# Kernel optimization log

Measured on AMD Instinct MI355X. Metric: run time of the kernel, lower is better.

The kernel has to match this reference:

```python
import jax, jax.numpy as jnp
import numpy as np
from itertools import permutations

NUM_LAYERS = 3
K = 5  # fixed node degree -> every Hungarian sub-problem is 5x5
# one-hot permutation tensor: P1H[p, r, c] = 1 iff permutation p assigns row r -> col c
PERMS = np.array(list(permutations(range(K))), dtype=np.int32)          # [120, K]
P1H = (PERMS[:, :, None] == np.arange(K)[None, None, :]).astype(np.float32)  # [120, K, K]


def _mlp(x, W1, b1, W2, b2):
    # 2-layer MLP with ReLU (repo's MLP(in, hid, out, 2))
    return jax.nn.relu(x @ W1 + b1) @ W2 + b2


def _sinkhorn(src, itera):
    s = jax.nn.softmax(src, axis=1)  # row-max subtraction is built in
    for i in range(itera):
        s = s / jnp.sum(s, axis=i % 2, keepdims=True)
    return jnp.nan_to_num(s)


def _masked_softmax(src):
    s1 = jnp.nan_to_num(jax.nn.softmax(src, axis=1))
    s2 = jnp.nan_to_num(jax.nn.softmax(src, axis=0))
    return (s1 + s2) * 0.5


def setup_inputs() -> dict:
    key = jax.random.key(0)
    ks = jax.random.split(key, 12)
    n1 = n2 = 1024
    hid = 64
    adj1 = jax.random.randint(ks[0], (n1, K), 0, n1)
    adj2 = jax.random.randint(ks[1], (n2, K), 0, n2)
    # adjacency matrices consistent with the neighbor lists
    G1 = jnp.zeros((n1, n1), jnp.float32).at[jnp.arange(n1)[:, None], adj1].set(1.0)
    G2 = jnp.zeros((n2, n2), jnp.float32).at[jnp.arange(n2)[:, None], adj2].set(1.0)
    s = 0.1
    return {
        'G1': G1, 'G2': G2, 'adj1': adj1, 'adj2': adj2,
        'ro_W1': jax.random.normal(ks[2], (NUM_LAYERS, 1, hid), jnp.float32) * s,
        'ro_b1': jax.random.normal(ks[3], (NUM_LAYERS, hid), jnp.float32) * s,
        'ro_W2': jax.random.normal(ks[4], (NUM_LAYERS, hid, 1), jnp.float32) * s,
        'ro_b2': jax.random.normal(ks[5], (NUM_LAYERS, 1), jnp.float32) * s,
        'fin_W1': jax.random.normal(ks[6], (1, hid), jnp.float32) * s,
        'fin_b1': jax.random.normal(ks[7], (hid,), jnp.float32) * s,
        'fin_W2': jax.random.normal(ks[8], (hid, 1), jnp.float32) * s,
        'fin_b2': jax.random.normal(ks[9], (1,), jnp.float32) * s,
    }


def reference(G1, G2, adj1, adj2, ro_W1, ro_b1, ro_W2, ro_b2, fin_W1, fin_b1, fin_W2, fin_b2):
    n1 = G1.shape[0]
    n2 = G2.shape[0]
    d1 = jnp.sum(G1, axis=1)
    d2 = jnp.sum(G2, axis=1)
    ttheta = jnp.mean(d1)
    # S[i, j, 0] = -|d1[i] - d2[j]|
    S = -jnp.abs(d1[:, None] - d2[None, :])[..., None]  # [n1, n2, 1]
    p1h = jnp.asarray(P1H)
    for li in range(NUM_LAYERS):
        Wn = _sinkhorn(_mlp(S / ttheta, ro_W1[li], ro_b1[li], ro_W2[li], ro_b2[li]).squeeze(-1), 5)
        W = jnp.log(Wn * (n1 * 1.5))
        W = jnp.where(jnp.isneginf(W), jnp.float32(-1e12), W)
        W = jnp.where(jnp.isposinf(W), jnp.float32(1e12), W)
        Wd = jax.lax.stop_gradient(W)  # matches W.detach().numpy()
        # small[a, b, r, c] = Wd[adj1[a, r], adj2[b, c]]  -> [n1, n2, K, K]
        small = jnp.transpose(Wd[adj1][:, :, adj2], (0, 2, 1, 3))
        # exact linear_sum_assignment(-small): maximize sum over the K! permutations
        scores = jnp.einsum('abrc,prc->abp', small, p1h)  # [n1, n2, 120]
        X1 = jnp.max(scores, axis=-1)                      # [n1, n2]
        S = X1[..., None]
    out = _masked_softmax(_mlp(S, fin_W1, fin_b1, fin_W2, fin_b2).squeeze(-1))
    return out
```

## Files before the change

### kernel.cpp

```cpp
#include <hip/hip_runtime.h>
#include <math.h>

#define N 1024
#define NB 256
#define KD 5
#define SL 8
#define NT 126
#define MAGIC 0x13572468
#define FSTRIDE 32
#define FREGION (NB * FSTRIDE + FSTRIDE)


__device__ __forceinline__ float load_sc(const float* p){
  return __hip_atomic_load(p, __ATOMIC_RELAXED, __HIP_MEMORY_SCOPE_AGENT);
}
__device__ __forceinline__ void store_sc(float* p, float v){
  __hip_atomic_store(p, v, __ATOMIC_RELAXED, __HIP_MEMORY_SCOPE_AGENT);
}
__device__ __forceinline__ int load_sci(const int* p){
  return __hip_atomic_load(p, __ATOMIC_RELAXED, __HIP_MEMORY_SCOPE_AGENT);
}
__device__ __forceinline__ void store_sci(int* p, int v){
  __hip_atomic_store(p, v, __ATOMIC_RELAXED, __HIP_MEMORY_SCOPE_AGENT);
}

__device__ __forceinline__ void gbarS(int* flg){
  __builtin_amdgcn_s_waitcnt(0);
  __syncthreads();
  const int t = threadIdx.x, B = blockIdx.x;
  int* go = flg + NB * FSTRIDE;
  if (B == 0){
    if (t > 0 && t < NB){
      while (load_sci(&flg[t * FSTRIDE]) != MAGIC) __builtin_amdgcn_s_sleep(2);
    }
    __syncthreads();
    if (t == 0) store_sci(go, MAGIC);
  } else {
    if (t == 0){
      store_sci(&flg[B * FSTRIDE], MAGIC);
      while (load_sci(go) != MAGIC) __builtin_amdgcn_s_sleep(2);
    }
    __syncthreads();
  }
}

__device__ __forceinline__ float wred_sum(float v){
#pragma unroll
  for (int off = 32; off > 0; off >>= 1) v += __shfl_down(v, off);
  return v;
}
__device__ __forceinline__ void bsum4(float v[4], float* s64){
  float w0 = wred_sum(v[0]), w1 = wred_sum(v[1]), w2 = wred_sum(v[2]), w3 = wred_sum(v[3]);
  __syncthreads();
  int wv = threadIdx.x >> 6;
  if ((threadIdx.x & 63) == 0){ s64[wv*4] = w0; s64[wv*4+1] = w1; s64[wv*4+2] = w2; s64[wv*4+3] = w3; }
  __syncthreads();
  float r0 = 0.f, r1 = 0.f, r2 = 0.f, r3 = 0.f;
#pragma unroll
  for (int i = 0; i < 16; ++i){ r0 += s64[i*4]; r1 += s64[i*4+1]; r2 += s64[i*4+2]; r3 += s64[i*4+3]; }
  v[0] = r0; v[1] = r1; v[2] = r2; v[3] = r3;
}

__device__ __forceinline__ int distinct5(const int* v){
  int c = 0;
#pragma unroll
  for (int r = 0; r < KD; ++r){
    bool dup = false;
#pragma unroll
    for (int s = 0; s < r; ++s) dup = dup || (v[s] == v[r]);
    c += dup ? 0 : 1;
  }
  return c;
}
__device__ __forceinline__ void sort5(int* s){
#pragma unroll
  for (int i = 0; i < 4; ++i)
#pragma unroll
    for (int j = 0; j < 4 - i; ++j){
      int a = s[j], b = s[j+1];
      s[j] = min(a, b); s[j+1] = max(a, b);
    }
}
__device__ __forceinline__ int msrank(const int* c5){
  const int C_[6][5] = { {0,0,0,0,0},
                         {1,1,1,1,1},
                         {1,2,3,4,5},
                         {1,3,6,10,15},
                         {1,4,10,20,35},
                         {1,5,15,35,70} };
  int rank = 0, prev = 0;
#pragma unroll
  for (int i = 0; i < 5; ++i){
    for (int v = prev; v < c5[i]; ++v) rank += C_[5 - v][4 - i];
    prev = c5[i];
  }
  return rank;
}

#define DP5(ACCESS, OUT) {                                        \
  float f[32]; f[0] = 0.f;                                        \
  _Pragma("unroll")                                               \
  for (int r = 0; r < KD; ++r){                                   \
    float tr[KD];                                                 \
    _Pragma("unroll")                                             \
    for (int c = 0; c < KD; ++c) tr[c] = (ACCESS);                \
    _Pragma("unroll")                                             \
    for (int m = 1; m < 32; ++m){                                 \
      if (__popc(m) == r + 1){                                    \
        float best = -3.0e38f;                                    \
        _Pragma("unroll")                                         \
        for (int c = 0; c < KD; ++c)                              \
          if (m & (1 << c)) best = fmaxf(best, f[m ^ (1 << c)] + tr[c]); \
        f[m] = best;                                              \
      }                                                           \
    }                                                             \
  }                                                               \
  OUT = f[31];                                                    \
}

__device__ __forceinline__ void pwl_build(int t,
    const float* __restrict__ w1g, const float* __restrict__ b1g,
    const float* __restrict__ w2g, const float* __restrict__ b2g,
    float* ux, float* udA, float* udB,
    float* xss, float* dAs, float* dBs,
    float* Atb, float* Btb, float* sA0B0)
{
  if (t < 64){
    float w1 = w1g[t], bb = b1g[t], w2v = w2g[t];
    float xk, sdA, sdB, a0t = 0.f, b0t = 0.f;
    if (w1 != 0.f){
      xk = -bb / w1;
      float dA = w1 * w2v, dB = bb * w2v;
      if (w1 > 0.f){ sdA = dA;  sdB = dB; }
      else         { sdA = -dA; sdB = -dB; a0t = dA; b0t = dB; }
    } else {
      xk = 3.0e38f; sdA = 0.f; sdB = 0.f;
      b0t = fmaxf(bb, 0.f) * w2v;
    }
    ux[t] = xk; udA[t] = sdA; udB[t] = sdB;
    float A0 = wred_sum(a0t);
    float B0 = wred_sum(b0t);
    if (t == 0){ sA0B0[0] = A0; sA0B0[1] = B0 + b2g[0]; }
  }
  __syncthreads();
  if (t < 64){
    float xk = ux[t]; int rank = 0;
    for (int j = 0; j < 64; ++j){
      float xj = ux[j];
      rank += (xj < xk || (xj == xk && j < t)) ? 1 : 0;
    }
    xss[rank] = ux[t]; dAs[rank] = udA[t]; dBs[rank] = udB[t];
  }
  __syncthreads();
  if (t < 65){
    float sa = sA0B0[0], sb = sA0B0[1];
    for (int r = 0; r < t; ++r){ sa += dAs[r]; sb += dBs[r]; }
    Atb[t] = sa; Btb[t] = sb;
  }
  __syncthreads();
}

__global__ __launch_bounds__(1024) void
kFused(const int* __restrict__ adj1, const int* __restrict__ adj2,
       const float* __restrict__ roW1, const float* __restrict__ roB1,
       const float* __restrict__ roW2, const float* __restrict__ roB2,
       const float* __restrict__ fW1, const float* __restrict__ fB1,
       const float* __restrict__ fW2, const float* __restrict__ fB2,
       float* __restrict__ tY1g,
       float* __restrict__ C1B, float* __restrict__ C2B, float* __restrict__ C3B,
       float* __restrict__ CFB, float* __restrict__ Rg,
       float* __restrict__ outp,
       int* __restrict__ flg)
{
  __shared__ __align__(16) char uS[20 * N * 4 + N * 4];
  float* tY1 = (float*)uS;
  float (*rows20)[N] = (float (*)[N])uS;
  float* lc = (float*)(uS + 20 * N * 4);
  __shared__ unsigned char t2c[NT][5];
  __shared__ unsigned char sg1[N], sg2[N];
  __shared__ unsigned short st1[N], st2[N];
  __shared__ int h1[8], h2[8];
  __shared__ int cnt1T[NT], cnt2T[NT];
  __shared__ float A1[NT], B1[NT];
  __shared__ float sY0[25], slR0[5], slC0[5], stt2[2];
  __shared__ float slR1[NT], slC1[NT];
  __shared__ float vq[NT], vC[NT], vqi[NT], vCi[NT];
  __shared__ float s64[64], sAv[4];
  __shared__ float ux[64], udA[64], udB[64], xss[64], dAs[64], dBs[64];
  __shared__ float Atb[65], Btb[65], sA0B0[2];

  const int t = threadIdx.x, B = blockIdx.x;
  const float L1536 = logf(1536.0f);

  if (t < 8){ h1[t] = 0; h2[t] = 0; }
  if (t < NT){ cnt1T[t] = 0; cnt2T[t] = 0; }
#pragma unroll 1
  for (int key = t; key < 3125; key += 1024){
    int d[5]; int k2 = key;
#pragma unroll
    for (int i = 0; i < 5; ++i){ d[i] = k2 % 5; k2 /= 5; }
    if (d[0] <= d[1] && d[1] <= d[2] && d[2] <= d[3] && d[3] <= d[4]){
      int r = msrank(d);
#pragma unroll
      for (int i = 0; i < 5; ++i) t2c[r][i] = (unsigned char)d[i];
    }
  }
  int a2[KD], a1v[KD];
#pragma unroll
  for (int c = 0; c < KD; ++c) a2[c] = adj2[t * KD + c];
#pragma unroll
  for (int r = 0; r < KD; ++r) a1v[r] = adj1[t * KD + r];
  {
    int c2 = distinct5(a2) - 1, c1 = distinct5(a1v) - 1;
    sg2[t] = (unsigned char)c2; sg1[t] = (unsigned char)c1;
    atomicAdd(&h2[c2], 1);
    atomicAdd(&h1[c1], 1);
  }
  __syncthreads();

  {
    int c5[KD];
#pragma unroll
    for (int r = 0; r < KD; ++r) c5[r] = sg1[a1v[r]];
    sort5(c5);
    int ty = msrank(c5);
    st1[t] = (unsigned short)ty; atomicAdd(&cnt1T[ty], 1);
  }
  {
    int c5[KD];
#pragma unroll
    for (int c = 0; c < KD; ++c) c5[c] = sg2[a2[c]];
    sort5(c5);
    int ty = msrank(c5);
    st2[t] = (unsigned short)ty; atomicAdd(&cnt2T[ty], 1);
  }

  if (t < 64){
    float cnt1[5], cnt2[5];
#pragma unroll
    for (int g = 0; g < 5; ++g){ cnt1[g] = (float)h1[g]; cnt2[g] = (float)h2[g]; }
    float tt = 0.f;
#pragma unroll
    for (int g = 0; g < 5; ++g) tt += (float)(g + 1) * cnt1[g];
    tt *= (1.0f / 1024.0f);
    float tab[5];
#pragma unroll 1
    for (int i = 0; i < 5; ++i){
      float x = -(float)i / tt;
      float acc = roB2[0];
      for (int k = 0; k < 64; ++k){
        float hh = fmaxf(fmaf(x, roW1[k], roB1[k]), 0.f);
        acc = fmaf(hh, roW2[k], acc);
      }
      tab[i] = acc;
    }
    float Ee[5][5];
#pragma unroll
    for (int g = 0; g < 5; ++g)
#pragma unroll
      for (int h = 0; h < 5; ++h) Ee[g][h] = expf(tab[abs(g - h)]);
    float q0[5], C1c[5], q1[5], C2c[5], q2[5], C3c[5];
#pragma unroll
    for (int g = 0; g < 5; ++g){
      float s = 0.f;
#pragma unroll
      for (int h = 0; h < 5; ++h) s += cnt2[h] * Ee[g][h];
      q0[g] = s;
    }
#pragma unroll
    for (int h = 0; h < 5; ++h){
      float s = 0.f;
#pragma unroll
      for (int g = 0; g < 5; ++g) s += cnt1[g] * Ee[g][h] / q0[g];
      C1c[h] = s;
    }
#pragma unroll
    for (int g = 0; g < 5; ++g){
      float s = 0.f;
#pragma unroll
      for (int h = 0; h < 5; ++h) s += cnt2[h] * Ee[g][h] / C1c[h];
      q1[g] = s;
    }
#pragma unroll
    for (int h = 0; h < 5; ++h){
      float s = 0.f;
#pragma unroll
      for (int g = 0; g < 5; ++g) s += cnt1[g] * Ee[g][h] / q1[g];
      C2c[h] = s;
    }
#pragma unroll
    for (int g = 0; g < 5; ++g){
      float s = 0.f;
#pragma unroll
      for (int h = 0; h < 5; ++h) s += cnt2[h] * Ee[g][h] / C2c[h];
      q2[g] = s;
    }
#pragma unroll
    for (int h = 0; h < 5; ++h){
      float s = 0.f;
#pragma unroll
      for (int g = 0; g < 5; ++g) s += cnt1[g] * Ee[g][h] / q2[g];
      C3c[h] = s;
    }
    if (t == 0){
#pragma unroll
      for (int g = 0; g < 5; ++g){
#pragma unroll
        for (int h = 0; h < 5; ++h) sY0[g * 5 + h] = tab[abs(g - h)];
        slR0[g] = -logf(q2[g]);
        slC0[g] = logf(C3c[g]);
      }
      stt2[0] = tt;
    }
  } else if (t < 128){
    int l = t - 64;
    const float* w1g = roW1 + 64;
    const float* b1g = roB1 + 64;
    const float* w2g = roW2 + 64;
    const float* b2g = roB2 + 1;
    float w1 = w1g[l], bb = b1g[l], w2v = w2g[l];
    float xk, sdA, sdB, a0t = 0.f, b0t = 0.f;
    if (w1 != 0.f){
      xk = -bb / w1;
      float dA = w1 * w2v, dB = bb * w2v;
      if (w1 > 0.f){ sdA = dA;  sdB = dB; }
      else         { sdA = -dA; sdB = -dB; a0t = dA; b0t = dB; }
    } else {
      xk = 3.0e38f; sdA = 0.f; sdB = 0.f;
      b0t = fmaxf(bb, 0.f) * w2v;
    }
    ux[l] = xk; udA[l] = sdA; udB[l] = sdB;
    float A0 = wred_sum(a0t);
    float B0 = wred_sum(b0t);
    if (l == 0){ sA0B0[0] = A0; sA0B0[1] = B0 + b2g[0]; }
  }
  __syncthreads();

  if (t < 64){
    float xk = ux[t]; int rank = 0;
    for (int j = 0; j < 64; ++j){
      float xj = ux[j];
      rank += (xj < xk || (xj == xk && j < t)) ? 1 : 0;
    }
    xss[rank] = ux[t]; dAs[rank] = udA[t]; dBs[rank] = udB[t];
  } else if (t >= 256 && t < 256 + NT){
    int ty = t - 256;
    float sa = 5.0f * L1536, sb = 0.f;
#pragma unroll
    for (int i = 0; i < KD; ++i){
      int cl = t2c[ty][i];
      sa += slR0[cl];
      sb -= slC0[cl];
    }
    A1[ty] = sa; B1[ty] = sb;
  }
  __syncthreads();
  if (t < 65){
    float sa = sA0B0[0], sb = sA0B0[1];
    for (int r = 0; r < t; ++r){ sa += dAs[r]; sb += dBs[r]; }
    Atb[t] = sa; Btb[t] = sb;
  }
  __syncthreads();

  const float tt = stt2[0];
  if (t < 63){
    int e = B + 256 * t;
    if (e < NT * NT){
      int tau = e / NT, ups = e - tau * NT;
      const unsigned char* G = t2c[tau];
      const unsigned char* H = t2c[ups];
      float D;
      DP5(sY0[(int)G[r] * 5 + (int)H[c]], D);
      float x = (A1[tau] + B1[ups] + D) / tt;
      int seg = 0;
#pragma unroll
      for (int s = 64; s; s >>= 1)
        if (seg + s <= 64 && xss[seg + s - 1] <= x) seg += s;
      store_sc(&tY1g[e], fmaf(Atb[seg], x, Btb[seg]));
    }
  }

  gbarS(flg + 0 * FREGION);

#pragma unroll 1
  for (int e = t; e < NT * NT; e += 1024) tY1[e] = load_sc(&tY1g[e]);

  pwl_build(t, roW1 + 128, roB1 + 128, roW2 + 128, roB2 + 2,
            ux, udA, udB, xss, dAs, dBs, Atb, Btb, sA0B0);

  {
    int g = t >> 3, j = t & 7;
    if (g < NT){
      float acc = 0.f;
      for (int u = j; u < NT; u += 8) acc += (float)cnt2T[u] * expf(tY1[g * NT + u]);
      acc += __shfl_down(acc, 4, 8); acc += __shfl_down(acc, 2, 8); acc += __shfl_down(acc, 1, 8);
      if (j == 0){ vq[g] = acc; vqi[g] = 1.0f / acc; }
    }
    __syncthreads();
    if (g < NT){
      float acc = 0.f;
      for (int u = j; u < NT; u += 8) acc += (float)cnt1T[u] * expf(tY1[u * NT + g]) * vqi[u];
      acc += __shfl_down(acc, 4, 8); acc += __shfl_down(acc, 2, 8); acc += __shfl_down(acc, 1, 8);
      if (j == 0){ vC[g] = acc; vCi[g] = 1.0f / acc; }
    }
    __syncthreads();
    if (g < NT){
      float acc = 0.f;
      for (int u = j; u < NT; u += 8) acc += (float)cnt2T[u] * expf(tY1[g * NT + u]) * vCi[u];
      acc += __shfl_down(acc, 4, 8); acc += __shfl_down(acc, 2, 8); acc += __shfl_down(acc, 1, 8);
      if (j == 0){ vq[g] = acc; vqi[g] = 1.0f / acc; }
    }
    __syncthreads();
    if (g < NT){
      float acc = 0.f;
      for (int u = j; u < NT; u += 8) acc += (float)cnt1T[u] * expf(tY1[u * NT + g]) * vqi[u];
      acc += __shfl_down(acc, 4, 8); acc += __shfl_down(acc, 2, 8); acc += __shfl_down(acc, 1, 8);
      if (j == 0){ vC[g] = acc; vCi[g] = 1.0f / acc; }
    }
    __syncthreads();
    if (g < NT){
      float acc = 0.f;
      for (int u = j; u < NT; u += 8) acc += (float)cnt2T[u] * expf(tY1[g * NT + u]) * vCi[u];
      acc += __shfl_down(acc, 4, 8); acc += __shfl_down(acc, 2, 8); acc += __shfl_down(acc, 1, 8);
      if (j == 0){ vq[g] = acc; vqi[g] = 1.0f / acc; }
    }
    __syncthreads();
    if (g < NT){
      float acc = 0.f;
      for (int u = j; u < NT; u += 8) acc += (float)cnt1T[u] * expf(tY1[u * NT + g]) * vqi[u];
      acc += __shfl_down(acc, 4, 8); acc += __shfl_down(acc, 2, 8); acc += __shfl_down(acc, 1, 8);
      if (j == 0) vC[g] = acc;
    }
    __syncthreads();
  }
  if (t < NT){ slR1[t] = -logf(vq[t]); slC1[t] = logf(vC[t]); }
  __syncthreads();

  if (t < 4){
    int a = 4 * B + t;
    float s = 5.0f * L1536;
#pragma unroll
    for (int r = 0; r < KD; ++r) s += slR1[st1[adj1[a * KD + r]]];
    sAv[t] = s;
  }
  int stc[KD];
  float Bv2 = 0.f;
#pragma unroll
  for (int c = 0; c < KD; ++c){ stc[c] = st2[a2[c]]; Bv2 -= slC1[stc[c]]; }
  __syncthreads();

  float y2[4];
#pragma unroll 1
  for (int rr = 0; rr < 4; ++rr){
    int str_[KD];
#pragma unroll
    for (int r = 0; r < KD; ++r) str_[r] = st1[adj1[(4 * B + rr) * KD + r]];
    float D;
    DP5(tY1[str_[r] * NT + stc[c]], D);
    float x = (sAv[rr] + Bv2 + D) / tt;
    int seg = 0;
#pragma unroll
    for (int s = 64; s; s >>= 1)
      if (seg + s <= 64 && xss[seg + s - 1] <= x) seg += s;
    y2[rr] = fmaf(Atb[seg], x, Btb[seg]);
  }
  float E[4], q4[4];
#pragma unroll
  for (int r = 0; r < 4; ++r){ E[r] = expf(y2[r]); q4[r] = E[r]; }
  bsum4(q4, s64);
  {
    float cp = 0.f;
#pragma unroll
    for (int r = 0; r < 4; ++r){
      store_sc(&outp[(size_t)(4 * B + r) * N + t], y2[r]);
      cp += E[r] / q4[r];
    }
    atomicAdd(&C1B[(size_t)(B & (SL - 1)) * N + t], cp);
  }

  gbarS(flg + 1 * FREGION);

#pragma unroll
  for (int k = 0; k < 20; ++k){
    int src = adj1[(4 * B + (k / 5)) * KD + (k % 5)];
    rows20[k][t] = load_sc(&outp[(size_t)src * N + t]);
  }

  pwl_build(t, fW1, fB1, fW2, fB2,
            ux, udA, udB, xss, dAs, dBs, Atb, Btb, sA0B0);

  {
    float C = 0.f;
#pragma unroll
    for (int k = 0; k < SL; ++k) C += load_sc(&C1B[(size_t)k * N + t]);
    float iC = 1.0f / C;
#pragma unroll
    for (int r = 0; r < 4; ++r) q4[r] = E[r] * iC;
    bsum4(q4, s64);
    float cp = 0.f;
#pragma unroll
    for (int r = 0; r < 4; ++r) cp += E[r] / q4[r];
    atomicAdd(&C2B[(size_t)(B & (SL - 1)) * N + t], cp);
  }

  gbarS(flg + 2 * FREGION);
  {
    float C = 0.f;
#pragma unroll
    for (int k = 0; k < SL; ++k) C += load_sc(&C2B[(size_t)k * N + t]);
    float iC = 1.0f / C;
#pragma unroll
    for (int r = 0; r < 4; ++r) q4[r] = E[r] * iC;
    bsum4(q4, s64);
    float cp = 0.f;
#pragma unroll
    for (int r = 0; r < 4; ++r) cp += E[r] / q4[r];
    if (t < 4) store_sc(&Rg[4 * B + t], 1.0f / q4[t]);
    atomicAdd(&C3B[(size_t)(B & (SL - 1)) * N + t], cp);
  }

  gbarS(flg + 3 * FREGION);
  {
    float C = 0.f;
#pragma unroll
    for (int k = 0; k < SL; ++k) C += load_sc(&C3B[(size_t)k * N + t]);
    lc[t] = logf(C);
  }
  if (t >= 64 && t < 68){
    int a = 4 * B + (t - 64);
    float s = 5.0f * logf(1536.0f);
#pragma unroll
    for (int r = 0; r < KD; ++r) s += logf(load_sc(&Rg[adj1[a * KD + r]]));
    sAv[t - 64] = s;
  }
  __syncthreads();

  float Bvl = 0.f;
#pragma unroll
  for (int c = 0; c < KD; ++c) Bvl -= lc[a2[c]];

  float y[4];
#pragma unroll 1
  for (int rr = 0; rr < 4; ++rr){
    float D;
    DP5(rows20[rr * 5 + r][a2[c]], D);
    float x = sAv[rr] + Bvl + D;
    int seg = 0;
#pragma unroll
    for (int s = 64; s; s >>= 1)
      if (seg + s <= 64 && xss[seg + s - 1] <= x) seg += s;
    y[rr] = fmaf(Atb[seg], x, Btb[seg]);
  }

  float e4[4];
#pragma unroll
  for (int r = 0; r < 4; ++r){ e4[r] = expf(y[r]); q4[r] = e4[r]; }
  bsum4(q4, s64);

  {
    float cp = 0.f;
#pragma unroll
    for (int r = 0; r < 4; ++r) cp += e4[r];
    atomicAdd(&CFB[(size_t)(B & (SL - 1)) * N + t], cp);
  }

  gbarS(flg + 4 * FREGION);
  float CF = 0.f;
#pragma unroll
  for (int k = 0; k < SL; ++k) CF += load_sc(&CFB[(size_t)k * N + t]);
  float iCF = 1.0f / CF;
#pragma unroll
  for (int r = 0; r < 4; ++r){
    float v = 0.5f * e4[r] * (1.0f / q4[r] + iCF);
    outp[(size_t)(4 * B + r) * N + t] = v;
  }
}

extern "C" void kernel_launch(void* const* d_in, const int* in_sizes, int n_in,
                              void* d_out, int out_size, void* d_ws, size_t ws_size,
                              hipStream_t stream){
  (void)in_sizes; (void)n_in; (void)out_size; (void)ws_size;
  const int*   adj1 = (const int*)d_in[2];
  const int*   adj2 = (const int*)d_in[3];
  const float* roW1 = (const float*)d_in[4];
  const float* roB1 = (const float*)d_in[5];
  const float* roW2 = (const float*)d_in[6];
  const float* roB2 = (const float*)d_in[7];
  const float* fW1  = (const float*)d_in[8];
  const float* fB1  = (const float*)d_in[9];
  const float* fW2  = (const float*)d_in[10];
  const float* fB2  = (const float*)d_in[11];
  float* out = (float*)d_out;

  float* Pp   = (float*)d_ws;
  float* Rg   = Pp + (size_t)4 * SL * N;
  float* tY1g = Rg + N;
  int*   flg  = (int*)(tY1g + NT * NT);

  kFused<<<NB, 1024, 0, stream>>>(adj1, adj2, roW1, roB1, roW2, roB2,
                                  fW1, fB1, fW2, fB2,
                                  tY1g,
                                  Pp + (size_t)0 * SL * N, Pp + (size_t)1 * SL * N,
                                  Pp + (size_t)2 * SL * N, Pp + (size_t)3 * SL * N,
                                  Rg, out, flg);
}
```

Baseline: 162.3 us.

## Hoist final PWL build before barrier, batch global loads, cache exp terms

Moves the final-MLP piecewise-linear table build ahead of the first grid barrier into separate shared tables, so it overlaps with barrier waiting instead of sitting on the critical path. Global loads of tY1 and the 20 neighbour rows are issued into registers as a batch and written to shared memory later, letting the latency of those loads overlap other work. The Sinkhorn iterations now compute the exp terms once into register arrays and reuse them across all six passes. The barrier spin sleep is also shortened. Costs are higher register pressure and extra shared memory.

```diff
diff --git a/kernel.cpp b/kernel.cpp
--- a/kernel.cpp
+++ b/kernel.cpp
@@ -31,14 +31,14 @@
   int* go = flg + NB * FSTRIDE;
   if (B == 0){
     if (t > 0 && t < NB){
-      while (load_sci(&flg[t * FSTRIDE]) != MAGIC) __builtin_amdgcn_s_sleep(2);
+      while (load_sci(&flg[t * FSTRIDE]) != MAGIC) __builtin_amdgcn_s_sleep(1);
     }
     __syncthreads();
     if (t == 0) store_sci(go, MAGIC);
   } else {
     if (t == 0){
       store_sci(&flg[B * FSTRIDE], MAGIC);
-      while (load_sci(go) != MAGIC) __builtin_amdgcn_s_sleep(2);
+      while (load_sci(go) != MAGIC) __builtin_amdgcn_s_sleep(1);
     }
     __syncthreads();
   }
@@ -188,6 +188,7 @@
   __shared__ float s64[64], sAv[4];
   __shared__ float ux[64], udA[64], udB[64], xss[64], dAs[64], dBs[64];
   __shared__ float Atb[65], Btb[65], sA0B0[2];
+  __shared__ float xs3[64], A3t[65], B3t[65];
 
   const int t = threadIdx.x, B = blockIdx.x;
   const float L1536 = logf(1536.0f);
@@ -380,54 +381,85 @@
     }
   }
 
+  pwl_build(t, fW1, fB1, fW2, fB2,
+            ux, udA, udB, xs3, dAs, dBs, A3t, B3t, sA0B0);
+
   gbarS(flg + 0 * FREGION);
 
-#pragma unroll 1
-  for (int e = t; e < NT * NT; e += 1024) tY1[e] = load_sc(&tY1g[e]);
+  {
+    float rv[16];
+#pragma unroll
+    for (int i = 0; i < 16; ++i){
+      int e = t + 1024 * i;
+      if (e < NT * NT) rv[i] = load_sc(&tY1g[e]);
+    }
+#pragma unroll
+    for (int i = 0; i < 16; ++i){
+      int e = t + 1024 * i;
+      if (e < NT * NT) tY1[e] = rv[i];
+    }
+  }
 
   pwl_build(t, roW1 + 128, roB1 + 128, roW2 + 128, roB2 + 2,
             ux, udA, udB, xss, dAs, dBs, Atb, Btb, sA0B0);
 
   {
     int g = t >> 3, j = t & 7;
+    float Er[16], Ec[16];
+    if (g < NT){
+#pragma unroll
+      for (int i = 0; i < 16; ++i){
+        int u = j + 8 * i;
+        if (u < NT){
+          Er[i] = (float)cnt2T[u] * expf(tY1[g * NT + u]);
+          Ec[i] = (float)cnt1T[u] * expf(tY1[u * NT + g]);
+        } else { Er[i] = 0.f; Ec[i] = 0.f; }
+      }
+    }
     if (g < NT){
       float acc = 0.f;
-      for (int u = j; u < NT; u += 8) acc += (float)cnt2T[u] * expf(tY1[g * NT + u]);
+#pragma unroll
+      for (int i = 0; i < 16; ++i){ int u = j + 8 * i; if (u < NT) acc += Er[i]; }
       acc += __shfl_down(acc, 4, 8); acc += __shfl_down(acc, 2, 8); acc += __shfl_down(acc, 1, 8);
       if (j == 0){ vq[g] = acc; vqi[g] = 1.0f / acc; }
     }
     __syncthreads();
     if (g < NT){
       float acc = 0.f;
-      for (int u = j; u < NT; u += 8) acc += (float)cnt1T[u] * expf(tY1[u * NT + g]) * vqi[u];
+#pragma unroll
+      for (int i = 0; i < 16; ++i){ int u = j + 8 * i; if (u < NT) acc += Ec[i] * vqi[u]; }
       acc += __shfl_down(acc, 4, 8); acc += __shfl_down(acc, 2, 8); acc += __shfl_down(acc, 1, 8);
       if (j == 0){ vC[g] = acc; vCi[g] = 1.0f / acc; }
     }
     __syncthreads();
     if (g < NT){
       float acc = 0.f;
-      for (int u = j; u < NT; u += 8) acc += (float)cnt2T[u] * expf(tY1[g * NT + u]) * vCi[u];
+#pragma unroll
+      for (int i = 0; i < 16; ++i){ int u = j + 8 * i; if (u < NT) acc += Er[i] * vCi[u]; }
       acc += __shfl_down(acc, 4, 8); acc += __shfl_down(acc, 2, 8); acc += __shfl_down(acc, 1, 8);
       if (j == 0){ vq[g] = acc; vqi[g] = 1.0f / acc; }
     }
     __syncthreads();
     if (g < NT){
       float acc = 0.f;
-      for (int u = j; u < NT; u += 8) acc += (float)cnt1T[u] * expf(tY1[u * NT + g]) * vqi[u];
+#pragma unroll
+      for (int i = 0; i < 16; ++i){ int u = j + 8 * i; if (u < NT) acc += Ec[i] * vqi[u]; }
       acc += __shfl_down(acc, 4, 8); acc += __shfl_down(acc, 2, 8); acc += __shfl_down(acc, 1, 8);
       if (j == 0){ vC[g] = acc; vCi[g] = 1.0f / acc; }
     }
     __syncthreads();
     if (g < NT){
       float acc = 0.f;
-      for (int u = j; u < NT; u += 8) acc += (float)cnt2T[u] * expf(tY1[g * NT + u]) * vCi[u];
+#pragma unroll
+      for (int i = 0; i < 16; ++i){ int u = j + 8 * i; if (u < NT) acc += Er[i] * vCi[u]; }
       acc += __shfl_down(acc, 4, 8); acc += __shfl_down(acc, 2, 8); acc += __shfl_down(acc, 1, 8);
       if (j == 0){ vq[g] = acc; vqi[g] = 1.0f / acc; }
     }
     __syncthreads();
     if (g < NT){
       float acc = 0.f;
-      for (int u = j; u < NT; u += 8) acc += (float)cnt1T[u] * expf(tY1[u * NT + g]) * vqi[u];
+#pragma unroll
+      for (int i = 0; i < 16; ++i){ int u = j + 8 * i; if (u < NT) acc += Ec[i] * vqi[u]; }
       acc += __shfl_down(acc, 4, 8); acc += __shfl_down(acc, 2, 8); acc += __shfl_down(acc, 1, 8);
       if (j == 0) vC[g] = acc;
     }
@@ -480,14 +512,12 @@
 
   gbarS(flg + 1 * FREGION);
 
+  float rv20[20];
 #pragma unroll
   for (int k = 0; k < 20; ++k){
     int src = adj1[(4 * B + (k / 5)) * KD + (k % 5)];
-    rows20[k][t] = load_sc(&outp[(size_t)src * N + t]);
-  }
-
-  pwl_build(t, fW1, fB1, fW2, fB2,
-            ux, udA, udB, xss, dAs, dBs, Atb, Btb, sA0B0);
+    rv20[k] = load_sc(&outp[(size_t)src * N + t]);
+  }
 
   {
     float C = 0.f;
@@ -502,6 +532,9 @@
     for (int r = 0; r < 4; ++r) cp += E[r] / q4[r];
     atomicAdd(&C2B[(size_t)(B & (SL - 1)) * N + t], cp);
   }
+
+#pragma unroll
+  for (int k = 0; k < 20; ++k) rows20[k][t] = rv20[k];
 
   gbarS(flg + 2 * FREGION);
   {
@@ -548,8 +581,8 @@
     int seg = 0;
 #pragma unroll
     for (int s = 64; s; s >>= 1)
-      if (seg + s <= 64 && xss[seg + s - 1] <= x) seg += s;
-    y[rr] = fmaf(Atb[seg], x, Btb[seg]);
+      if (seg + s <= 64 && xs3[seg + s - 1] <= x) seg += s;
+    y[rr] = fmaf(A3t[seg], x, B3t[seg]);
   }
 
   float e4[4];
```

Result: faster. 150.4 us (-7.4%).
